# Performance work log

Hardware: AMD Instinct MI355X
Metric: run time of the kernel (lower is better)

The kernel has to match this reference:

```python
import jax, jax.numpy as jnp
from jax import lax
import numpy as np

BN_INV = 1.0 / np.sqrt(1.0 + 1e-5)  # eval-mode BatchNorm with running mean 0, var 1


def gather_points(x, idx):
    # x: [B, N, C]; idx: [B, ...] int -> [B, ..., C]
    bi = jnp.arange(x.shape[0]).reshape((x.shape[0],) + (1,) * (idx.ndim - 1))
    return x[bi, idx]


def fps(xyz, npoint):
    # furthest point sampling starting at index 0. xyz: [B, N, 3] -> [B, npoint] int32
    B, N, _ = xyz.shape

    def step(carry, _):
        dist, last = carry
        lx = jnp.take_along_axis(xyz, last[:, None, None], axis=1)  # [B,1,3]
        d = jnp.sum((xyz - lx) ** 2, axis=-1)                       # [B,N]
        dist = jnp.minimum(dist, d)
        nxt = jnp.argmax(dist, axis=-1).astype(jnp.int32)
        return (dist, nxt), nxt

    first = jnp.zeros((B,), jnp.int32)
    dist0 = jnp.full((B, N), 1e10, xyz.dtype)
    _, rest = lax.scan(step, (dist0, first), None, length=npoint - 1)
    return jnp.concatenate([first[None], rest], axis=0).T  # [B, npoint]


def ball_query(radius, nsample, xyz, new_xyz):
    # first nsample points (in index order) within radius of each query; pad with first hit
    N = xyz.shape[1]
    d2 = jnp.sum((new_xyz[:, :, None, :] - xyz[:, None, :, :]) ** 2, axis=-1)  # [B,S,N]
    mask = d2 < radius * radius
    key = jnp.where(mask, jnp.arange(N, dtype=jnp.int32), N)
    idx_sorted = jnp.sort(key, axis=-1)[..., :nsample]                          # [B,S,ns]
    cnt = jnp.sum(mask, axis=-1, keepdims=True)                                 # [B,S,1]
    idx = jnp.where(jnp.arange(nsample) < cnt, idx_sorted, idx_sorted[..., :1])
    return jnp.minimum(idx, N - 1)


def bn_relu(x, gamma, beta):
    # eval-mode BN (running mean 0 / var 1) + ReLU; channels on the last axis
    return jax.nn.relu(x * (gamma * BN_INV) + beta)


def sa_module(xyz, feats, npoint, radius, nsample, layers):
    # xyz [B,N,3], feats [B,C,N] -> (new_xyz [B,S,3], new_feats [B,Cout,S])
    fidx = fps(xyz, npoint)
    new_xyz = gather_points(xyz, fidx)                      # [B,S,3]
    gidx = ball_query(radius, nsample, xyz, new_xyz)        # [B,S,ns]
    g_xyz = gather_points(xyz, gidx) - new_xyz[:, :, None, :]   # [B,S,ns,3]
    g_feat = gather_points(jnp.swapaxes(feats, 1, 2), gidx)     # [B,S,ns,C]
    h = jnp.concatenate([g_xyz, g_feat], axis=-1)               # use_xyz=True
    for (w, g, b) in layers:                                    # shared MLP (1x1 conv2d+BN+ReLU)
        h = bn_relu(jnp.einsum('bsnc,oc->bsno', h, w), g, b)
    return new_xyz, jnp.swapaxes(jnp.max(h, axis=2), 1, 2)      # max-pool over nsample


def fp_module(unk_xyz, kn_xyz, unk_feats, kn_feats, layers):
    # three-NN weighted interpolation (squared distances, as the CUDA op) + unit conv MLP
    d2 = jnp.sum((unk_xyz[:, :, None, :] - kn_xyz[:, None, :, :]) ** 2, axis=-1)
    neg, idx = lax.top_k(-d2, 3)                 # 3 nearest known points
    w = 1.0 / (-neg + 1e-8)
    w = w / jnp.sum(w, axis=-1, keepdims=True)   # [B,Nu,3]
    kf = gather_points(jnp.swapaxes(kn_feats, 1, 2), idx)       # [B,Nu,3,C]
    interp = jnp.sum(kf * w[..., None], axis=2)                 # [B,Nu,C]
    h = jnp.concatenate([interp, jnp.swapaxes(unk_feats, 1, 2)], axis=-1)
    for (wt, g, b) in layers:
        h = bn_relu(jnp.einsum('bnc,oc->bno', h, wt), g, b)
    return jnp.swapaxes(h, 1, 2)                                # [B,Cout,Nu]


def setup_inputs() -> dict:
    key = jax.random.key(0)
    it = iter(jax.random.split(key, 80))
    B, N = 16, 4096
    d = {
        'xyz': jax.random.uniform(next(it), (B, N, 3), jnp.float32) * 0.3,
        'feats': jax.random.normal(next(it), (B, N, 3), jnp.float32),
    }
    specs = {'sa1': [(6, 64), (64, 128)], 'sa2': [(131, 128), (128, 256)],
             'sa3': [(259, 256), (256, 512)], 'fp3': [(768, 256), (256, 256)],
             'fp2': [(384, 128), (128, 128)], 'fp1': [(131, 128), (128, 128)]}
    for name, layers in specs.items():
        for i, (ci, co) in enumerate(layers):
            d[f'{name}_w{i}'] = jax.random.normal(next(it), (co, ci), jnp.float32) / np.sqrt(ci)
            d[f'{name}_g{i}'] = 1.0 + 0.1 * jax.random.normal(next(it), (co,), jnp.float32)
            d[f'{name}_b{i}'] = 0.1 * jax.random.normal(next(it), (co,), jnp.float32)
    d['fin_w'] = jax.random.normal(next(it), (512, 128), jnp.float32) / np.sqrt(128.0)
    d['fin_b'] = 0.1 * jax.random.normal(next(it), (512,), jnp.float32)
    d['fin_g'] = 1.0 + 0.1 * jax.random.normal(next(it), (512,), jnp.float32)
    d['fin_be'] = 0.1 * jax.random.normal(next(it), (512,), jnp.float32)
    return d


def reference(xyz, feats,
              sa1_w0, sa1_g0, sa1_b0, sa1_w1, sa1_g1, sa1_b1,
              sa2_w0, sa2_g0, sa2_b0, sa2_w1, sa2_g1, sa2_b1,
              sa3_w0, sa3_g0, sa3_b0, sa3_w1, sa3_g1, sa3_b1,
              fp3_w0, fp3_g0, fp3_b0, fp3_w1, fp3_g1, fp3_b1,
              fp2_w0, fp2_g0, fp2_b0, fp2_w1, fp2_g1, fp2_b1,
              fp1_w0, fp1_g0, fp1_b0, fp1_w1, fp1_g1, fp1_b1,
              fin_w, fin_b, fin_g, fin_be):
    f0 = jnp.swapaxes(feats, 1, 2)  # [B,3,N], channel-first like the torch module
    l1x, l1f = sa_module(xyz, f0, 256, 0.04, 16,
                         [(sa1_w0, sa1_g0, sa1_b0), (sa1_w1, sa1_g1, sa1_b1)])
    l2x, l2f = sa_module(l1x, l1f, 64, 0.08, 16,
                         [(sa2_w0, sa2_g0, sa2_b0), (sa2_w1, sa2_g1, sa2_b1)])
    l3x, l3f = sa_module(l2x, l2f, 16, 0.16, 16,
                         [(sa3_w0, sa3_g0, sa3_b0), (sa3_w1, sa3_g1, sa3_b1)])
    l2f = fp_module(l2x, l3x, l2f, l3f, [(fp3_w0, fp3_g0, fp3_b0), (fp3_w1, fp3_g1, fp3_b1)])
    l1f = fp_module(l1x, l2x, l1f, l2f, [(fp2_w0, fp2_g0, fp2_b0), (fp2_w1, fp2_g1, fp2_b1)])
    l0f = fp_module(xyz, l1x, f0, l1f, [(fp1_w0, fp1_g0, fp1_b0), (fp1_w1, fp1_g1, fp1_b1)])
    # final Conv1d(128->512, bias) + BN + ReLU
    h = jnp.einsum('bcn,oc->bon', l0f, fin_w) + fin_b[None, :, None]
    h = jax.nn.relu(h * (fin_g * BN_INV)[None, :, None] + fin_be[None, :, None])
    B, C, N = h.shape
    return jnp.swapaxes(h, 1, 2).reshape(B * N, C)  # un-batched per-point features
```

## Files before the change

### kernel.cpp

```cpp
#include <hip/hip_runtime.h>

#define DEVI __device__ __forceinline__
typedef unsigned long long u64;

static constexpr float BN_INV_F = 0.9999950000374997f;

DEVI float d2rn(float ax, float ay, float az, float bx, float by, float bz) {
    float dx = __fsub_rn(ax, bx), dy = __fsub_rn(ay, by), dz = __fsub_rn(az, bz);
    return __fadd_rn(__fadd_rn(__fmul_rn(dx, dx), __fmul_rn(dy, dy)), __fmul_rn(dz, dz));
}

DEVI u64 shfl_xor_u64(u64 x, int m) {
    unsigned lo = (unsigned)x, hi = (unsigned)(x >> 32);
    lo = (unsigned)__shfl_xor((int)lo, m, 64);
    hi = (unsigned)__shfl_xor((int)hi, m, 64);
    return ((u64)hi << 32) | lo;
}
DEVI u64 umin64(u64 a, u64 b) { return a < b ? a : b; }
DEVI u64 umax64(u64 a, u64 b) { return a > b ? a : b; }

template <int N, int NPOINT, int BS>
DEVI void fps_impl(const float* __restrict__ xyz, int* __restrict__ fidx) {
    constexpr int PPT = N / BS;
    constexpr int NW = BS / 64;
    __shared__ float4 xs4[N];
    __shared__ u64 wmax[2][NW > 1 ? NW : 1];
    const int t = threadIdx.x, b = blockIdx.x, lane = t & 63, wv = t >> 6;
    const float* xb = xyz + (size_t)b * N * 3;
    for (int p = t; p < N; p += BS)
        xs4[p] = make_float4(xb[p * 3], xb[p * 3 + 1], xb[p * 3 + 2], 0.f);
    if (t == 0) fidx[b * NPOINT] = 0;
    __syncthreads();
    float px[PPT], py[PPT], pz[PPT], dist[PPT];
#pragma unroll
    for (int i = 0; i < PPT; ++i) {
        float4 v = xs4[i * BS + t];
        px[i] = v.x; py[i] = v.y; pz[i] = v.z;
        dist[i] = 1e10f;
    }
    float4 q0 = xs4[0];
    float qx = q0.x, qy = q0.y, qz = q0.z;
    for (int it = 1; it < NPOINT; ++it) {
        u64 best = 0ull;
#pragma unroll
        for (int i = 0; i < PPT; ++i) {
            float d = d2rn(px[i], py[i], pz[i], qx, qy, qz);
            float nd = fminf(dist[i], d);
            dist[i] = nd;
            u64 pk = ((u64)__float_as_uint(nd) << 32) |
                     (unsigned)(0xFFFFFFFFu - (unsigned)(i * BS + t));
            best = umax64(best, pk);
        }
#pragma unroll
        for (int m = 1; m < 64; m <<= 1) best = umax64(best, shfl_xor_u64(best, m));
        if constexpr (NW > 1) {
            if (lane == 0) wmax[it & 1][wv] = best;
            __syncthreads();
            u64 m2 = wmax[it & 1][lane & (NW - 1)];
#pragma unroll
            for (int m = 1; m < NW; m <<= 1) m2 = umax64(m2, shfl_xor_u64(m2, m));
            best = m2;
        }
        int p = (int)(0xFFFFFFFFu - (unsigned)best);
        float4 qv = xs4[p];
        qx = qv.x; qy = qv.y; qz = qv.z;
        if (t == 0) fidx[b * NPOINT + it] = p;
    }
}

__global__ __launch_bounds__(512) void fps1_kernel(const float* __restrict__ x, int* __restrict__ f) { fps_impl<4096, 256, 512>(x, f); }
__global__ __launch_bounds__(64)  void fps2_kernel(const float* __restrict__ x, int* __restrict__ f) { fps_impl<256, 64, 64>(x, f); }
__global__ __launch_bounds__(64)  void fps3_kernel(const float* __restrict__ x, int* __restrict__ f) { fps_impl<64, 16, 64>(x, f); }

template <int TR, int XSTR, int KMAIN, int CIM, int CIF, int MOFF, int CO, int MODE,
          bool SIDE, int SOFF, int OSTR>
DEVI void gemm_phase(float* __restrict__ Xs, float* __restrict__ Ws,
                     const float* __restrict__ W,
                     const float* __restrict__ sA, const float* __restrict__ sB,
                     const float* __restrict__ fbias,
                     float* __restrict__ gout, int r0,
                     unsigned* __restrict__ mp, const float* __restrict__ side, int t) {
    constexpr int RT = TR / 16;
    constexpr int NCOL = (CO / 16 < 8) ? (CO / 16) : 8;
    constexpr int ROWS = 16 * NCOL;
    constexpr int CC = CO / ROWS;
    constexpr int NCH = KMAIN / 8;
    constexpr int NQ = CC * NCH;
    constexpr int PRE = ROWS / 32;
    constexpr int XSTR4 = XSTR / 4;
    constexpr int AC = (MODE == 0) ? CC : 1;
    const int tx = t & 15, ty = t >> 4;
    const int swz = ty & 3;
    float acc[AC][RT][NCOL];
    if constexpr (MODE == 0) {
#pragma unroll
        for (int a = 0; a < AC; ++a)
#pragma unroll
            for (int r = 0; r < RT; ++r)
#pragma unroll
                for (int i = 0; i < NCOL; ++i) acc[a][r][i] = 0.f;
    }
    float pre[PRE];
#pragma unroll
    for (int i = 0; i < PRE; ++i) {
        int e = t + 256 * i, row = e >> 3, kk = e & 7;
        pre[i] = (kk < CIM) ? W[(size_t)row * CIF + MOFF + kk] : 0.f;
    }
#pragma unroll
    for (int i = 0; i < PRE; ++i) {
        int e = t + 256 * i;
        Ws[(e >> 3) * 12 + (e & 7)] = pre[i];
    }
#pragma unroll
    for (int cc = 0; cc < CC; ++cc) {
        if constexpr (MODE != 0) {
#pragma unroll
            for (int r = 0; r < RT; ++r)
#pragma unroll
                for (int i = 0; i < NCOL; ++i) acc[0][r][i] = 0.f;
        }
        for (int kc = 0; kc < NCH; ++kc) {
            const int qq = cc * NCH + kc, buf = kc & 1;
            __syncthreads();
            if (qq + 1 < NQ) {
                const int cn = (qq + 1) / NCH, kn = ((qq + 1) % NCH) * 8;
#pragma unroll
                for (int i = 0; i < PRE; ++i) {
                    int e = t + 256 * i, row = e >> 3, k = kn + (e & 7);
                    pre[i] = (k < CIM) ? W[(size_t)(cn * ROWS + row) * CIF + MOFF + k] : 0.f;
                }
            }
            const float* wsb = Ws + buf * (ROWS * 12);
#pragma unroll
            for (int k4i = 0; k4i < 2; ++k4i) {
                const int c4 = kc * 2 + k4i;
                float4 wv[NCOL];
#pragma unroll
                for (int i = 0; i < NCOL; ++i)
                    wv[i] = *(const float4*)&wsb[(tx + 16 * i) * 12 + k4i * 4];
                float4 xv[RT];
#pragma unroll
                for (int r = 0; r < RT; ++r)
                    xv[r] = *(const float4*)&Xs[((ty * RT + r) * XSTR4 + (c4 ^ swz)) * 4];
#pragma unroll
                for (int r = 0; r < RT; ++r)
#pragma unroll
                    for (int i = 0; i < NCOL; ++i) {
                        const int a = (MODE == 0) ? cc : 0;
                        acc[a][r][i] = fmaf(xv[r].x, wv[i].x, acc[a][r][i]);
                        acc[a][r][i] = fmaf(xv[r].y, wv[i].y, acc[a][r][i]);
                        acc[a][r][i] = fmaf(xv[r].z, wv[i].z, acc[a][r][i]);
                        acc[a][r][i] = fmaf(xv[r].w, wv[i].w, acc[a][r][i]);
                    }
            }
            if (qq + 1 < NQ) {
                float* wsn = Ws + (buf ^ 1) * (ROWS * 12);
#pragma unroll
                for (int i = 0; i < PRE; ++i) {
                    int e = t + 256 * i;
                    wsn[(e >> 3) * 12 + (e & 7)] = pre[i];
                }
            }
        }
        if constexpr (MODE == 1) {
#pragma unroll
            for (int i = 0; i < NCOL; ++i) {
                int c = cc * ROWS + tx + 16 * i;
                float bia = fbias ? fbias[c] : 0.f;
                float sc = sA[c] * BN_INV_F, be = sB[c];
#pragma unroll
                for (int r = 0; r < RT; ++r) {
                    float val = fmaxf(fmaf(acc[0][r][i] + bia, sc, be), 0.f);
                    gout[(size_t)(r0 + ty * RT + r) * OSTR + c] = val;
                }
            }
        } else if constexpr (MODE == 2) {
#pragma unroll
            for (int i = 0; i < NCOL; ++i) {
                int c = cc * ROWS + tx + 16 * i;
                float sc = sA[c] * BN_INV_F, bb = sB[c];
#pragma unroll
                for (int r = 0; r < RT; ++r) {
                    float val = fmaxf(fmaf(acc[0][r][i], sc, bb), 0.f);
                    atomicMax(&mp[((ty * RT + r) >> 4) * CO + c], __float_as_uint(val));
                }
            }
        }
    }
    if constexpr (MODE == 0) {
        if constexpr (SIDE) {
#pragma unroll
            for (int cc = 0; cc < AC; ++cc)
#pragma unroll
                for (int i = 0; i < NCOL; ++i) {
                    int c = cc * ROWS + tx + 16 * i;
#pragma unroll
                    for (int j = 0; j < 3; ++j) {
                        float wj = W[(size_t)c * CIF + SOFF + j];
#pragma unroll
                        for (int r = 0; r < RT; ++r)
                            acc[cc][r][i] = fmaf(side[(ty * RT + r) * 3 + j], wj,
                                                 acc[cc][r][i]);
                    }
                }
        }
        __syncthreads();
#pragma unroll
        for (int cc = 0; cc < AC; ++cc)
#pragma unroll
            for (int i = 0; i < NCOL; ++i) {
                int c = cc * ROWS + tx + 16 * i;
                float sc = sA[c] * BN_INV_F, bb = sB[c];
#pragma unroll
                for (int r = 0; r < RT; ++r) {
                    int row = ty * RT + r;
                    Xs[(row * XSTR4 + ((c >> 2) ^ swz)) * 4 + (c & 3)] =
                        fmaxf(fmaf(acc[cc][r][i], sc, bb), 0.f);
                }
            }
        __syncthreads();
    }
}

template <int N, int S, int CIN, int C1, int C2, int TR, bool USE_SIDE>
DEVI void sa_impl(const float* __restrict__ xyz, const float* __restrict__ feats,
                  const int* __restrict__ fidx,
                  const float* __restrict__ w0, const float* __restrict__ g0, const float* __restrict__ b0,
                  const float* __restrict__ w1, const float* __restrict__ g1, const float* __restrict__ b1,
                  float* __restrict__ oxyz, float* __restrict__ ofeat, float r2) {
    constexpr int QPB = TR / 16;
    constexpr int CIF = 3 + CIN;
    constexpr int KMAIN = USE_SIDE ? CIN : 16;
    constexpr int XSTR = (KMAIN > C1) ? KMAIN : C1;
    constexpr int XSTR4 = XSTR / 4;
    constexpr int RT = TR / 16;
    __shared__ __align__(16) float Xs[TR * XSTR];
    __shared__ __align__(16) float Ws[2 * 128 * 12];
    __shared__ int ids[QPB][16];
    __shared__ float qp[QPB][3];
    __shared__ unsigned mp[QPB * C2];
    __shared__ float side[USE_SIDE ? TR * 3 : 4];
    const int t = threadIdx.x, lane = t & 63, wv = t >> 6;
    const int q0 = blockIdx.x * QPB;
    for (int q = wv; q < QPB; q += 4) {
        const int sq = q0 + q, bb = sq / S;
        const float* xb = xyz + (size_t)bb * N * 3;
        const int qi = fidx[sq];
        const float qx = xb[qi * 3], qy = xb[qi * 3 + 1], qz = xb[qi * 3 + 2];
        if (lane == 0) {
            qp[q][0] = qx; qp[q][1] = qy; qp[q][2] = qz;
            float* op = oxyz + (size_t)sq * 3;
            op[0] = qx; op[1] = qy; op[2] = qz;
        }
        int base = 0;
        for (int seg = 0; seg < N; seg += 64) {
            const int p = seg + lane;
            float d = d2rn(xb[p * 3], xb[p * 3 + 1], xb[p * 3 + 2], qx, qy, qz);
            bool hit = d < r2;
            u64 mask = __ballot(hit);
            int before = (int)__popcll(mask & ((1ull << lane) - 1ull));
            if (hit && base + before < 16) ids[q][base + before] = p;
            base += (int)__popcll(mask);
            if (base >= 16) break;
        }
        if (lane == 0) {
            int cnt = base < 16 ? base : 16;
            int first = ids[q][0];
            for (int r = cnt; r < 16; ++r) ids[q][r] = first;
        }
    }
    __syncthreads();
    if constexpr (!USE_SIDE) {
        for (int e = t; e < TR * 16; e += 256) {
            int j = e >> 4, c = e & 15;
            int q = j >> 4, p = ids[q][j & 15];
            int bb = (q0 + q) / S;
            float v = 0.f;
            if (c < 3) v = __fsub_rn(xyz[((size_t)bb * N + p) * 3 + c], qp[q][c]);
            else if (c < 6) v = feats[((size_t)bb * N + p) * CIN + (c - 3)];
            Xs[(j * XSTR4 + ((c >> 2) ^ ((j / RT) & 3))) * 4 + (c & 3)] = v;
        }
    } else {
        constexpr int C4N = CIN / 4;
        for (int e = t; e < TR * C4N; e += 256) {
            int j = e / C4N, c4 = e % C4N;
            int q = j >> 4, p = ids[q][j & 15];
            int bb = (q0 + q) / S;
            float4 v = *(const float4*)&feats[((size_t)bb * N + p) * CIN + c4 * 4];
            *(float4*)&Xs[(j * XSTR4 + (c4 ^ ((j / RT) & 3))) * 4] = v;
        }
        for (int e = t; e < TR * 3; e += 256) {
            int j = e / 3, c = e % 3;
            int q = j >> 4, p = ids[q][j & 15];
            int bb = (q0 + q) / S;
            side[e] = __fsub_rn(xyz[((size_t)bb * N + p) * 3 + c], qp[q][c]);
        }
    }
    for (int e = t; e < QPB * C2; e += 256) mp[e] = 0u;
    gemm_phase<TR, XSTR, KMAIN, (USE_SIDE ? CIN : 6), CIF, (USE_SIDE ? 3 : 0),
               C1, 0, USE_SIDE, 0, 0>(Xs, Ws, w0, g0, b0, nullptr, nullptr, 0,
                                      nullptr, side, t);
    gemm_phase<TR, XSTR, C1, C1, C1, 0, C2, 2, false, 0, 0>(
        Xs, Ws, w1, g1, b1, nullptr, nullptr, 0, mp, nullptr, t);
    __syncthreads();
    for (int e = t; e < QPB * C2; e += 256)
        ofeat[(size_t)q0 * C2 + e] = __uint_as_float(mp[e]);
}

#define SA_ARGS const float* __restrict__ xyz, const float* __restrict__ feats, \
                const int* __restrict__ fidx, \
                const float* __restrict__ w0, const float* __restrict__ g0, const float* __restrict__ b0, \
                const float* __restrict__ w1, const float* __restrict__ g1, const float* __restrict__ b1, \
                float* __restrict__ oxyz, float* __restrict__ ofeat, float r2
__global__ __launch_bounds__(256) void sa1_kernel(SA_ARGS) {
    sa_impl<4096, 256, 3, 64, 128, 64, false>(xyz, feats, fidx, w0, g0, b0, w1, g1, b1, oxyz, ofeat, r2);
}
__global__ __launch_bounds__(256) void sa2_kernel(SA_ARGS) {
    sa_impl<256, 64, 128, 128, 256, 64, true>(xyz, feats, fidx, w0, g0, b0, w1, g1, b1, oxyz, ofeat, r2);
}
__global__ __launch_bounds__(256) void sa3_kernel(SA_ARGS) {
    sa_impl<64, 16, 256, 256, 512, 16, true>(xyz, feats, fidx, w0, g0, b0, w1, g1, b1, oxyz, ofeat, r2);
}

template <int M, int CK, int CU, int C1, int C2, int TR>
DEVI void fp_impl(const float* __restrict__ uxyz, const float* __restrict__ kxyz,
                  const float* __restrict__ ufeat, const float* __restrict__ kfeat,
                  const float* __restrict__ w0, const float* __restrict__ g0, const float* __restrict__ b0,
                  const float* __restrict__ w1, const float* __restrict__ g1, const float* __restrict__ b1,
                  float* __restrict__ out, int NU) {
    constexpr int CH = CK + CU;
    constexpr int XSTR = CH;
    constexpr int XSTR4 = XSTR / 4;
    constexpr int RT = TR / 16;
    __shared__ __align__(16) float Xs[TR * XSTR];
    __shared__ __align__(16) float Ws[2 * 128 * 12];
    __shared__ float kxs[M * 3];
    const int t = threadIdx.x, lane = t & 63, wv = t >> 6;
    const int r0 = blockIdx.x * TR;
    const int b = r0 / NU;
    for (int e = t; e < M * 3; e += 256) kxs[e] = kxyz[(size_t)b * M * 3 + e];
    __syncthreads();
    for (int j = wv; j < TR; j += 4) {
        const int r = r0 + j;
        const int sw = (j / RT) & 3;
        const float* up = uxyz + (size_t)r * 3;
        float ux = up[0], uy = up[1], uz = up[2];
        u64 a0 = ~0ull, a1 = ~0ull, a2 = ~0ull;
        for (int k = lane; k < M; k += 64) {
            float d = d2rn(kxs[k * 3], kxs[k * 3 + 1], kxs[k * 3 + 2], ux, uy, uz);
            u64 key = ((u64)__float_as_uint(d) << 32) | (unsigned)k;
            if (key < a0)      { a2 = a1; a1 = a0; a0 = key; }
            else if (key < a1) { a2 = a1; a1 = key; }
            else if (key < a2) { a2 = key; }
        }
#pragma unroll
        for (int m = 1; m < 64; m <<= 1) {
            u64 b0k = shfl_xor_u64(a0, m), b1k = shfl_xor_u64(a1, m), b2k = shfl_xor_u64(a2, m);
            u64 c0 = umin64(a0, b0k);
            u64 c1 = umin64(umax64(a0, b0k), umin64(a1, b1k));
            u64 c2 = umin64(umin64(umax64(a1, b0k), umax64(a0, b1k)), umin64(a2, b2k));
            a0 = c0; a1 = c1; a2 = c2;
        }
        int s0 = (int)(unsigned)a0, s1 = (int)(unsigned)a1, s2 = (int)(unsigned)a2;
        float d0 = __uint_as_float((unsigned)(a0 >> 32));
        float d1 = __uint_as_float((unsigned)(a1 >> 32));
        float dd2 = __uint_as_float((unsigned)(a2 >> 32));
        float wa = 1.0f / (d0 + 1e-8f), wb = 1.0f / (d1 + 1e-8f), wc = 1.0f / (dd2 + 1e-8f);
        float sum = (wa + wb) + wc;
        wa /= sum; wb /= sum; wc /= sum;
        const float* kb = kfeat + (size_t)b * M * CK;
        for (int c4 = lane; c4 < CK / 4; c4 += 64) {
            float4 va = *(const float4*)(kb + (size_t)s0 * CK + c4 * 4);
            float4 vb = *(const float4*)(kb + (size_t)s1 * CK + c4 * 4);
            float4 vc = *(const float4*)(kb + (size_t)s2 * CK + c4 * 4);
            float4 rr;
            rr.x = va.x * wa + vb.x * wb + vc.x * wc;
            rr.y = va.y * wa + vb.y * wb + vc.y * wc;
            rr.z = va.z * wa + vb.z * wb + vc.z * wc;
            rr.w = va.w * wa + vb.w * wb + vc.w * wc;
            *(float4*)&Xs[(j * XSTR4 + (c4 ^ sw)) * 4] = rr;
        }
        for (int c4 = CK / 4 + lane; c4 < CH / 4; c4 += 64) {
            float4 v = *(const float4*)&ufeat[(size_t)r * CU + (c4 * 4 - CK)];
            *(float4*)&Xs[(j * XSTR4 + (c4 ^ sw)) * 4] = v;
        }
    }
    gemm_phase<TR, XSTR, CH, CH, CH, 0, C1, 0, false, 0, 0>(
        Xs, Ws, w0, g0, b0, nullptr, nullptr, 0, nullptr, nullptr, t);
    gemm_phase<TR, XSTR, C1, C1, C1, 0, C2, 1, false, 0, C2>(
        Xs, Ws, w1, g1, b1, nullptr, out, r0, nullptr, nullptr, t);
}

#define FP_ARGS const float* __restrict__ uxyz, const float* __restrict__ kxyz, \
                const float* __restrict__ ufeat, const float* __restrict__ kfeat, \
                const float* __restrict__ w0, const float* __restrict__ g0, const float* __restrict__ b0, \
                const float* __restrict__ w1, const float* __restrict__ g1, const float* __restrict__ b1, \
                float* __restrict__ out, int NU
__global__ __launch_bounds__(256) void fp3_kernel(FP_ARGS) {
    fp_impl<16, 512, 256, 256, 256, 16>(uxyz, kxyz, ufeat, kfeat, w0, g0, b0, w1, g1, b1, out, NU);
}
__global__ __launch_bounds__(256) void fp2_kernel(FP_ARGS) {
    fp_impl<64, 256, 128, 128, 128, 16>(uxyz, kxyz, ufeat, kfeat, w0, g0, b0, w1, g1, b1, out, NU);
}

__global__ __launch_bounds__(256) void fp1_mlp_kernel(
    const float* __restrict__ uxyz, const float* __restrict__ kxyz,
    const float* __restrict__ ufeat3, const float* __restrict__ kfeat,
    const float* __restrict__ w0, const float* __restrict__ g0, const float* __restrict__ b0,
    const float* __restrict__ w1, const float* __restrict__ g1, const float* __restrict__ b1,
    float* __restrict__ out) {
    constexpr int TR = 128, M = 256, CK = 128;
    __shared__ __align__(16) float Xs[TR * 128];
    __shared__ __align__(16) float Ws[2 * 128 * 12];
    __shared__ float side[TR * 3];
    __shared__ float wgt2[TR * 2];
    __shared__ unsigned pidx[TR];
    const int t = threadIdx.x;
    const int r0 = blockIdx.x * TR;
    const int b = r0 >> 12;
    for (int e = t; e < TR * 3; e += 256) side[e] = ufeat3[(size_t)r0 * 3 + e];
    const int g = t >> 2, sub = t & 3;
    const float* kb3 = kxyz + (size_t)b * M * 3;
    for (int row = g; row < TR; row += 64) {
        const float* up = uxyz + (size_t)(r0 + row) * 3;
        float ux = up[0], uy = up[1], uz = up[2];
        u64 a0 = ~0ull, a1 = ~0ull, a2 = ~0ull;
        for (int k = sub; k < M; k += 4) {
            float d = d2rn(kb3[k * 3], kb3[k * 3 + 1], kb3[k * 3 + 2], ux, uy, uz);
            u64 key = ((u64)__float_as_uint(d) << 32) | (unsigned)k;
            if (key < a0)      { a2 = a1; a1 = a0; a0 = key; }
            else if (key < a1) { a2 = a1; a1 = key; }
            else if (key < a2) { a2 = key; }
        }
#pragma unroll
        for (int m = 1; m < 4; m <<= 1) {
            u64 b0k = shfl_xor_u64(a0, m), b1k = shfl_xor_u64(a1, m), b2k = shfl_xor_u64(a2, m);
            u64 c0 = umin64(a0, b0k);
            u64 c1 = umin64(umax64(a0, b0k), umin64(a1, b1k));
            u64 c2 = umin64(umin64(umax64(a1, b0k), umax64(a0, b1k)), umin64(a2, b2k));
            a0 = c0; a1 = c1; a2 = c2;
        }
        if (sub == 0) {
            unsigned s0 = (unsigned)a0 & 255u, s1 = (unsigned)a1 & 255u, s2 = (unsigned)a2 & 255u;
            float d0 = __uint_as_float((unsigned)(a0 >> 32));
            float d1 = __uint_as_float((unsigned)(a1 >> 32));
            float dd2 = __uint_as_float((unsigned)(a2 >> 32));
            float wa = 1.0f / (d0 + 1e-8f), wb = 1.0f / (d1 + 1e-8f), wc = 1.0f / (dd2 + 1e-8f);
            float sum = (wa + wb) + wc;
            wa /= sum; wb /= sum;
            pidx[row] = s0 | (s1 << 8) | (s2 << 16);
            wgt2[row * 2] = wa; wgt2[row * 2 + 1] = wb;
        }
    }
    __syncthreads();
    const float* kfb = kfeat + (size_t)b * M * CK;
    for (int e = t; e < TR * 32; e += 256) {
        int j = e >> 5, c4 = e & 31;
        unsigned u = pidx[j];
        int s0 = u & 255, s1 = (u >> 8) & 255, s2 = (u >> 16) & 255;
        float wa = wgt2[j * 2], wb = wgt2[j * 2 + 1], wc = 1.0f - wa - wb;
        float4 va = *(const float4*)(kfb + (size_t)s0 * CK + c4 * 4);
        float4 vb = *(const float4*)(kfb + (size_t)s1 * CK + c4 * 4);
        float4 vc = *(const float4*)(kfb + (size_t)s2 * CK + c4 * 4);
        float4 rr;
        rr.x = va.x * wa + vb.x * wb + vc.x * wc;
        rr.y = va.y * wa + vb.y * wb + vc.y * wc;
        rr.z = va.z * wa + vb.z * wb + vc.z * wc;
        rr.w = va.w * wa + vb.w * wb + vc.w * wc;
        *(float4*)&Xs[(j * 32 + (c4 ^ ((j >> 3) & 3))) * 4] = rr;
    }
    gemm_phase<TR, 128, 128, 128, 131, 0, 128, 0, true, 128, 0>(
        Xs, Ws, w0, g0, b0, nullptr, nullptr, 0, nullptr, side, t);
    gemm_phase<TR, 128, 128, 128, 128, 0, 128, 1, false, 0, 512>(
        Xs, Ws, w1, g1, b1, nullptr, out, r0, nullptr, nullptr, t);
}

__global__ __launch_bounds__(256) void fin_kernel(
    float* io,
    const float* __restrict__ fw, const float* __restrict__ fb,
    const float* __restrict__ fg, const float* __restrict__ fbe) {
    __shared__ __align__(16) float Xs[128 * 128];
    __shared__ __align__(16) float Ws[2 * 128 * 12];
    const int t = threadIdx.x, tx = t & 15, ty = t >> 4;
    const int r0 = blockIdx.x * 128;
    const int swz = ty & 3;
    for (int e = t; e < 128 * 32; e += 256) {
        int j = e >> 5, c4 = e & 31;
        float4 v = *(const float4*)&io[(size_t)(r0 + j) * 512 + c4 * 4];
        *(float4*)&Xs[(j * 32 + (c4 ^ ((j >> 3) & 3))) * 4] = v;
    }
    for (int nt = 0; nt < 4; ++nt) {
        const int c0 = nt * 128;
        float acc[8][8];
#pragma unroll
        for (int r = 0; r < 8; ++r)
#pragma unroll
            for (int i = 0; i < 8; ++i) acc[r][i] = 0.f;
        float wpre[4];
#pragma unroll
        for (int i = 0; i < 4; ++i) {
            int e = t + 256 * i, row = e >> 3, kk = e & 7;
            wpre[i] = fw[(size_t)(c0 + row) * 128 + kk];
        }
#pragma unroll
        for (int i = 0; i < 4; ++i) {
            int e = t + 256 * i;
            Ws[(e >> 3) * 12 + (e & 7)] = wpre[i];
        }
        for (int kc = 0; kc < 16; ++kc) {
            const int buf = kc & 1;
            __syncthreads();
            if (kc < 15) {
                const int kn = (kc + 1) * 8;
#pragma unroll
                for (int i = 0; i < 4; ++i) {
                    int e = t + 256 * i, row = e >> 3, kk = e & 7;
                    wpre[i] = fw[(size_t)(c0 + row) * 128 + kn + kk];
                }
            }
            const float* wsb = Ws + buf * 1536;
#pragma unroll
            for (int k4i = 0; k4i < 2; ++k4i) {
                const int c4 = kc * 2 + k4i;
                float4 wv[8];
#pragma unroll
                for (int i = 0; i < 8; ++i)
                    wv[i] = *(const float4*)&wsb[(tx + 16 * i) * 12 + k4i * 4];
                float4 xv[8];
#pragma unroll
                for (int r = 0; r < 8; ++r)
                    xv[r] = *(const float4*)&Xs[((ty * 8 + r) * 32 + (c4 ^ swz)) * 4];
#pragma unroll
                for (int r = 0; r < 8; ++r)
#pragma unroll
                    for (int i = 0; i < 8; ++i) {
                        acc[r][i] = fmaf(xv[r].x, wv[i].x, acc[r][i]);
                        acc[r][i] = fmaf(xv[r].y, wv[i].y, acc[r][i]);
                        acc[r][i] = fmaf(xv[r].z, wv[i].z, acc[r][i]);
                        acc[r][i] = fmaf(xv[r].w, wv[i].w, acc[r][i]);
                    }
            }
            if (kc < 15) {
                float* wsn = Ws + (buf ^ 1) * 1536;
#pragma unroll
                for (int i = 0; i < 4; ++i) {
                    int e = t + 256 * i;
                    wsn[(e >> 3) * 12 + (e & 7)] = wpre[i];
                }
            }
        }
#pragma unroll
        for (int i = 0; i < 8; ++i) {
            int c = c0 + tx + 16 * i;
            float bia = fb[c], sc = fg[c] * BN_INV_F, be = fbe[c];
#pragma unroll
            for (int r = 0; r < 8; ++r) {
                float val = fmaxf(fmaf(acc[r][i] + bia, sc, be), 0.f);
                io[(size_t)(r0 + ty * 8 + r) * 512 + c] = val;
            }
        }
    }
}

extern "C" void kernel_launch(void* const* d_in, const int* in_sizes, int n_in,
                              void* d_out, int out_size, void* d_ws, size_t ws_size,
                              hipStream_t stream) {
    (void)in_sizes; (void)n_in; (void)out_size; (void)ws_size;
    const float* xyz   = (const float*)d_in[0];
    const float* feats = (const float*)d_in[1];
    const float* sa1_w0 = (const float*)d_in[2];
    const float* sa1_g0 = (const float*)d_in[3];
    const float* sa1_b0 = (const float*)d_in[4];
    const float* sa1_w1 = (const float*)d_in[5];
    const float* sa1_g1 = (const float*)d_in[6];
    const float* sa1_b1 = (const float*)d_in[7];
    const float* sa2_w0 = (const float*)d_in[8];
    const float* sa2_g0 = (const float*)d_in[9];
    const float* sa2_b0 = (const float*)d_in[10];
    const float* sa2_w1 = (const float*)d_in[11];
    const float* sa2_g1 = (const float*)d_in[12];
    const float* sa2_b1 = (const float*)d_in[13];
    const float* sa3_w0 = (const float*)d_in[14];
    const float* sa3_g0 = (const float*)d_in[15];
    const float* sa3_b0 = (const float*)d_in[16];
    const float* sa3_w1 = (const float*)d_in[17];
    const float* sa3_g1 = (const float*)d_in[18];
    const float* sa3_b1 = (const float*)d_in[19];
    const float* fp3_w0 = (const float*)d_in[20];
    const float* fp3_g0 = (const float*)d_in[21];
    const float* fp3_b0 = (const float*)d_in[22];
    const float* fp3_w1 = (const float*)d_in[23];
    const float* fp3_g1 = (const float*)d_in[24];
    const float* fp3_b1 = (const float*)d_in[25];
    const float* fp2_w0 = (const float*)d_in[26];
    const float* fp2_g0 = (const float*)d_in[27];
    const float* fp2_b0 = (const float*)d_in[28];
    const float* fp2_w1 = (const float*)d_in[29];
    const float* fp2_g1 = (const float*)d_in[30];
    const float* fp2_b1 = (const float*)d_in[31];
    const float* fp1_w0 = (const float*)d_in[32];
    const float* fp1_g0 = (const float*)d_in[33];
    const float* fp1_b0 = (const float*)d_in[34];
    const float* fp1_w1 = (const float*)d_in[35];
    const float* fp1_g1 = (const float*)d_in[36];
    const float* fp1_b1 = (const float*)d_in[37];
    const float* fin_w  = (const float*)d_in[38];
    const float* fin_b  = (const float*)d_in[39];
    const float* fin_g  = (const float*)d_in[40];
    const float* fin_be = (const float*)d_in[41];

    float* ws = (float*)d_ws;
    float* l1x  = ws;
    float* l1f  = l1x + 12288;
    float* l2x  = l1f + 524288;
    float* l2f  = l2x + 3072;
    float* l3x  = l2f + 262144;
    float* l3f  = l3x + 768;
    float* l2fb = l3f + 131072;
    float* l1fb = l2fb + 262144;
    int* fidx1 = (int*)(l1fb + 524288);
    int* fidx2 = fidx1 + 4096;
    int* fidx3 = fidx2 + 1024;

    const float R2_1 = (float)(0.04 * 0.04);
    const float R2_2 = (float)(0.08 * 0.08);
    const float R2_3 = (float)(0.16 * 0.16);

    fps1_kernel<<<16, 512, 0, stream>>>(xyz, fidx1);
    sa1_kernel<<<1024, 256, 0, stream>>>(
        xyz, feats, fidx1, sa1_w0, sa1_g0, sa1_b0, sa1_w1, sa1_g1, sa1_b1,
        l1x, l1f, R2_1);

    fps2_kernel<<<16, 64, 0, stream>>>(l1x, fidx2);
    sa2_kernel<<<256, 256, 0, stream>>>(
        l1x, l1f, fidx2, sa2_w0, sa2_g0, sa2_b0, sa2_w1, sa2_g1, sa2_b1,
        l2x, l2f, R2_2);

    fps3_kernel<<<16, 64, 0, stream>>>(l2x, fidx3);
    sa3_kernel<<<256, 256, 0, stream>>>(
        l2x, l2f, fidx3, sa3_w0, sa3_g0, sa3_b0, sa3_w1, sa3_g1, sa3_b1,
        l3x, l3f, R2_3);

    fp3_kernel<<<64, 256, 0, stream>>>(
        l2x, l3x, l2f, l3f, fp3_w0, fp3_g0, fp3_b0, fp3_w1, fp3_g1, fp3_b1,
        l2fb, 64);

    fp2_kernel<<<256, 256, 0, stream>>>(
        l1x, l2x, l1f, l2fb, fp2_w0, fp2_g0, fp2_b0, fp2_w1, fp2_g1, fp2_b1,
        l1fb, 256);

    fp1_mlp_kernel<<<512, 256, 0, stream>>>(
        xyz, l1x, feats, l1fb, fp1_w0, fp1_g0, fp1_b0, fp1_w1, fp1_g1, fp1_b1,
        (float*)d_out);

    fin_kernel<<<512, 256, 0, stream>>>(
        (float*)d_out, fin_w, fin_b, fin_g, fin_be);
}
```

Measured before the change: 810.5 us.

## Fuse final conv into fp1 MLP kernel and streamline FPS argmax

The final 128->512 conv+BN+ReLU now runs as a third gemm phase inside the fp1 kernel. The fp1 second layer keeps its output in shared memory instead of writing it to the output buffer, which removes a kernel launch and a global write and read of the intermediate. FPS now tracks the per-thread argmax as a float/index pair and packs a 64-bit key only once before the wave reduction. FPS1 also runs with 256 threads instead of 512, giving more points per thread and fewer waves per barrier. The risk is that fp1 now carries the whole 512-column output phase in one block, which could lower occupancy or increase register use.

```diff
diff --git a/kernel.cpp b/kernel.cpp
--- a/kernel.cpp
+++ b/kernel.cpp
@@ -41,16 +41,16 @@
     float4 q0 = xs4[0];
     float qx = q0.x, qy = q0.y, qz = q0.z;
     for (int it = 1; it < NPOINT; ++it) {
-        u64 best = 0ull;
+        float bestd = -1.f;
+        unsigned bestidx = 0u;
 #pragma unroll
         for (int i = 0; i < PPT; ++i) {
             float d = d2rn(px[i], py[i], pz[i], qx, qy, qz);
             float nd = fminf(dist[i], d);
             dist[i] = nd;
-            u64 pk = ((u64)__float_as_uint(nd) << 32) |
-                     (unsigned)(0xFFFFFFFFu - (unsigned)(i * BS + t));
-            best = umax64(best, pk);
-        }
+            if (nd > bestd) { bestd = nd; bestidx = (unsigned)(i * BS + t); }
+        }
+        u64 best = ((u64)__float_as_uint(bestd) << 32) | (0xFFFFFFFFu - bestidx);
 #pragma unroll
         for (int m = 1; m < 64; m <<= 1) best = umax64(best, shfl_xor_u64(best, m));
         if constexpr (NW > 1) {
@@ -68,7 +68,7 @@
     }
 }
 
-__global__ __launch_bounds__(512) void fps1_kernel(const float* __restrict__ x, int* __restrict__ f) { fps_impl<4096, 256, 512>(x, f); }
+__global__ __launch_bounds__(256) void fps1_kernel(const float* __restrict__ x, int* __restrict__ f) { fps_impl<4096, 256, 256>(x, f); }
 __global__ __launch_bounds__(64)  void fps2_kernel(const float* __restrict__ x, int* __restrict__ f) { fps_impl<256, 64, 64>(x, f); }
 __global__ __launch_bounds__(64)  void fps3_kernel(const float* __restrict__ x, int* __restrict__ f) { fps_impl<64, 16, 64>(x, f); }
 
@@ -403,11 +403,13 @@
     fp_impl<64, 256, 128, 128, 128, 16>(uxyz, kxyz, ufeat, kfeat, w0, g0, b0, w1, g1, b1, out, NU);
 }
 
-__global__ __launch_bounds__(256) void fp1_mlp_kernel(
+__global__ __launch_bounds__(256) void fp1_fused_kernel(
     const float* __restrict__ uxyz, const float* __restrict__ kxyz,
     const float* __restrict__ ufeat3, const float* __restrict__ kfeat,
     const float* __restrict__ w0, const float* __restrict__ g0, const float* __restrict__ b0,
     const float* __restrict__ w1, const float* __restrict__ g1, const float* __restrict__ b1,
+    const float* __restrict__ fw, const float* __restrict__ fb,
+    const float* __restrict__ fg, const float* __restrict__ fbe,
     float* __restrict__ out) {
     constexpr int TR = 128, M = 256, CK = 128;
     __shared__ __align__(16) float Xs[TR * 128];
@@ -471,95 +473,10 @@
     }
     gemm_phase<TR, 128, 128, 128, 131, 0, 128, 0, true, 128, 0>(
         Xs, Ws, w0, g0, b0, nullptr, nullptr, 0, nullptr, side, t);
-    gemm_phase<TR, 128, 128, 128, 128, 0, 128, 1, false, 0, 512>(
-        Xs, Ws, w1, g1, b1, nullptr, out, r0, nullptr, nullptr, t);
-}
-
-__global__ __launch_bounds__(256) void fin_kernel(
-    float* io,
-    const float* __restrict__ fw, const float* __restrict__ fb,
-    const float* __restrict__ fg, const float* __restrict__ fbe) {
-    __shared__ __align__(16) float Xs[128 * 128];
-    __shared__ __align__(16) float Ws[2 * 128 * 12];
-    const int t = threadIdx.x, tx = t & 15, ty = t >> 4;
-    const int r0 = blockIdx.x * 128;
-    const int swz = ty & 3;
-    for (int e = t; e < 128 * 32; e += 256) {
-        int j = e >> 5, c4 = e & 31;
-        float4 v = *(const float4*)&io[(size_t)(r0 + j) * 512 + c4 * 4];
-        *(float4*)&Xs[(j * 32 + (c4 ^ ((j >> 3) & 3))) * 4] = v;
-    }
-    for (int nt = 0; nt < 4; ++nt) {
-        const int c0 = nt * 128;
-        float acc[8][8];
-#pragma unroll
-        for (int r = 0; r < 8; ++r)
-#pragma unroll
-            for (int i = 0; i < 8; ++i) acc[r][i] = 0.f;
-        float wpre[4];
-#pragma unroll
-        for (int i = 0; i < 4; ++i) {
-            int e = t + 256 * i, row = e >> 3, kk = e & 7;
-            wpre[i] = fw[(size_t)(c0 + row) * 128 + kk];
-        }
-#pragma unroll
-        for (int i = 0; i < 4; ++i) {
-            int e = t + 256 * i;
-            Ws[(e >> 3) * 12 + (e & 7)] = wpre[i];
-        }
-        for (int kc = 0; kc < 16; ++kc) {
-            const int buf = kc & 1;
-            __syncthreads();
-            if (kc < 15) {
-                const int kn = (kc + 1) * 8;
-#pragma unroll
-                for (int i = 0; i < 4; ++i) {
-                    int e = t + 256 * i, row = e >> 3, kk = e & 7;
-                    wpre[i] = fw[(size_t)(c0 + row) * 128 + kn + kk];
-                }
-            }
-            const float* wsb = Ws + buf * 1536;
-#pragma unroll
-            for (int k4i = 0; k4i < 2; ++k4i) {
-                const int c4 = kc * 2 + k4i;
-                float4 wv[8];
-#pragma unroll
-                for (int i = 0; i < 8; ++i)
-                    wv[i] = *(const float4*)&wsb[(tx + 16 * i) * 12 + k4i * 4];
-                float4 xv[8];
-#pragma unroll
-                for (int r = 0; r < 8; ++r)
-                    xv[r] = *(const float4*)&Xs[((ty * 8 + r) * 32 + (c4 ^ swz)) * 4];
-#pragma unroll
-                for (int r = 0; r < 8; ++r)
-#pragma unroll
-                    for (int i = 0; i < 8; ++i) {
-                        acc[r][i] = fmaf(xv[r].x, wv[i].x, acc[r][i]);
-                        acc[r][i] = fmaf(xv[r].y, wv[i].y, acc[r][i]);
-                        acc[r][i] = fmaf(xv[r].z, wv[i].z, acc[r][i]);
-                        acc[r][i] = fmaf(xv[r].w, wv[i].w, acc[r][i]);
-                    }
-            }
-            if (kc < 15) {
-                float* wsn = Ws + (buf ^ 1) * 1536;
-#pragma unroll
-                for (int i = 0; i < 4; ++i) {
-                    int e = t + 256 * i;
-                    wsn[(e >> 3) * 12 + (e & 7)] = wpre[i];
-                }
-            }
-        }
-#pragma unroll
-        for (int i = 0; i < 8; ++i) {
-            int c = c0 + tx + 16 * i;
-            float bia = fb[c], sc = fg[c] * BN_INV_F, be = fbe[c];
-#pragma unroll
-            for (int r = 0; r < 8; ++r) {
-                float val = fmaxf(fmaf(acc[r][i] + bia, sc, be), 0.f);
-                io[(size_t)(r0 + ty * 8 + r) * 512 + c] = val;
-            }
-        }
-    }
+    gemm_phase<TR, 128, 128, 128, 128, 0, 128, 0, false, 0, 0>(
+        Xs, Ws, w1, g1, b1, nullptr, nullptr, 0, nullptr, nullptr, t);
+    gemm_phase<TR, 128, 128, 128, 128, 0, 512, 1, false, 0, 512>(
+        Xs, Ws, fw, fg, fbe, fb, out, r0, nullptr, nullptr, t);
 }
 
 extern "C" void kernel_launch(void* const* d_in, const int* in_sizes, int n_in,
@@ -626,7 +543,7 @@
     const float R2_2 = (float)(0.08 * 0.08);
     const float R2_3 = (float)(0.16 * 0.16);
 
-    fps1_kernel<<<16, 512, 0, stream>>>(xyz, fidx1);
+    fps1_kernel<<<16, 256, 0, stream>>>(xyz, fidx1);
     sa1_kernel<<<1024, 256, 0, stream>>>(
         xyz, feats, fidx1, sa1_w0, sa1_g0, sa1_b0, sa1_w1, sa1_g1, sa1_b1,
         l1x, l1f, R2_1);
@@ -649,10 +566,7 @@
         l1x, l2x, l1f, l2fb, fp2_w0, fp2_g0, fp2_b0, fp2_w1, fp2_g1, fp2_b1,
         l1fb, 256);
 
-    fp1_mlp_kernel<<<512, 256, 0, stream>>>(
+    fp1_fused_kernel<<<512, 256, 0, stream>>>(
         xyz, l1x, feats, l1fb, fp1_w0, fp1_g0, fp1_b0, fp1_w1, fp1_g1, fp1_b1,
-        (float*)d_out);
-
-    fin_kernel<<<512, 256, 0, stream>>>(
-        (float*)d_out, fin_w, fin_b, fin_g, fin_be);
-}
+        fin_w, fin_b, fin_g, fin_be, (float*)d_out);
+}
```

Result: slower. 883.4 us (+9.0%).
